# Performance work log

Hardware: AMD Instinct MI355X
Metric: run time of the kernel (lower is better)

The kernel has to match this reference:

```python
import jax, jax.numpy as jnp
import numpy as np

N, F_IN, F_OUT = 8192, 512, 256

def setup_inputs() -> dict:
    key = jax.random.key(0)
    kx, kW, ka = jax.random.split(key, 3)
    x = jax.random.normal(kx, (N, F_IN), dtype=jnp.float32)
    adj = jnp.ones((N, N), dtype=jnp.float32)  # accepted but unused by the original forward
    # nn.Linear(in, out, bias=False) stores weight as [out, in]
    W = jax.random.normal(kW, (F_OUT, F_IN), dtype=jnp.float32) * 0.02
    # nn.Linear(2*out, 1, bias=False) -> attention vector of length 2*F_OUT
    a = jax.random.normal(ka, (2 * F_OUT,), dtype=jnp.float32) * 0.02
    return {"x": x, "adj": adj, "W": W, "a": a}

def reference(x, adj, W, a):
    # h = W(x): [N, F_OUT]
    h = x @ W.T
    # Original concatenates [h_i, h_j] for all pairs (O(N^2 * 2F) memory) and
    # applies linear a. Since a is linear, e_ij = a1.h_i + a2.h_j -> broadcast add.
    a_src, a_dst = a[:F_OUT], a[F_OUT:]
    e = (h @ a_src)[:, None] + (h @ a_dst)[None, :]  # [N, N]
    attention = jax.nn.softmax(e, axis=1)             # row-wise over neighbors j
    h_prime = attention @ h                           # [N, F_OUT]
    return h_prime
```

## Files before the change

### kernel.cpp

```cpp
#include <hip/hip_runtime.h>
#include <math.h>

#define NN 8192
#define FIN 512
#define FOUT 256

__global__ __launch_bounds__(256) void gemm_xwT(const float* __restrict__ A,
                                                const float* __restrict__ B,
                                                float* __restrict__ C) {
    const int K = FIN;
    __shared__ float As[32][68];
    __shared__ float Bs[32][68];

    const int bx = blockIdx.x;
    const int by = blockIdx.y;
    const int tid = threadIdx.x;
    const int tx = tid & 15;
    const int ty = tid >> 4;

    const int lr = tid >> 3;
    const int lk = (tid & 7) << 2;

    const float* Ab = A + (size_t)(by * 64) * K;
    const float* Bb = B + (size_t)(bx * 64) * K;

    float acc[4][4] = {};

    for (int k0 = 0; k0 < K; k0 += 32) {
        float4 a0 = *(const float4*)(Ab + (size_t)lr * K + k0 + lk);
        float4 a1 = *(const float4*)(Ab + (size_t)(lr + 32) * K + k0 + lk);
        float4 b0 = *(const float4*)(Bb + (size_t)lr * K + k0 + lk);
        float4 b1 = *(const float4*)(Bb + (size_t)(lr + 32) * K + k0 + lk);
        __syncthreads();
        As[lk + 0][lr] = a0.x; As[lk + 1][lr] = a0.y;
        As[lk + 2][lr] = a0.z; As[lk + 3][lr] = a0.w;
        As[lk + 0][lr + 32] = a1.x; As[lk + 1][lr + 32] = a1.y;
        As[lk + 2][lr + 32] = a1.z; As[lk + 3][lr + 32] = a1.w;
        Bs[lk + 0][lr] = b0.x; Bs[lk + 1][lr] = b0.y;
        Bs[lk + 2][lr] = b0.z; Bs[lk + 3][lr] = b0.w;
        Bs[lk + 0][lr + 32] = b1.x; Bs[lk + 1][lr + 32] = b1.y;
        Bs[lk + 2][lr + 32] = b1.z; Bs[lk + 3][lr + 32] = b1.w;
        __syncthreads();
        #pragma unroll
        for (int kk = 0; kk < 32; ++kk) {
            float4 av = *(const float4*)&As[kk][ty << 2];
            float4 bv = *(const float4*)&Bs[kk][tx << 2];
            float am[4] = {av.x, av.y, av.z, av.w};
            float bn[4] = {bv.x, bv.y, bv.z, bv.w};
            #pragma unroll
            for (int i = 0; i < 4; ++i)
                #pragma unroll
                for (int j = 0; j < 4; ++j)
                    acc[i][j] = fmaf(am[i], bn[j], acc[i][j]);
        }
    }

    const int m0 = by * 64 + (ty << 2);
    const int n0 = bx * 64 + (tx << 2);
    #pragma unroll
    for (int i = 0; i < 4; ++i) {
        float4 o = make_float4(acc[i][0], acc[i][1], acc[i][2], acc[i][3]);
        *(float4*)(C + (size_t)(m0 + i) * FOUT + n0) = o;
    }
}

__global__ __launch_bounds__(256) void row_dot(const float* __restrict__ h,
                                               const float* __restrict__ a_dst,
                                               float* __restrict__ d) {
    const int lane = threadIdx.x & 63;
    const int wave = threadIdx.x >> 6;
    const int row = blockIdx.x * 4 + wave;
    float4 hv = *(const float4*)(h + (size_t)row * FOUT + (lane << 2));
    float4 av = *(const float4*)(a_dst + (lane << 2));
    float s = hv.x * av.x + hv.y * av.y + hv.z * av.z + hv.w * av.w;
    #pragma unroll
    for (int off = 32; off; off >>= 1) s += __shfl_down(s, off);
    if (lane == 0) d[row] = s;
}

__global__ __launch_bounds__(1024) void softmax_stats(const float* __restrict__ d,
                                                      float* __restrict__ stats) {
    __shared__ float red[16];
    const int tid = threadIdx.x;
    const int lane = tid & 63;
    const int wid = tid >> 6;

    const float4* dp = (const float4*)d + (size_t)tid * 2;
    float4 v0 = dp[0], v1 = dp[1];

    float m = fmaxf(fmaxf(fmaxf(v0.x, v0.y), fmaxf(v0.z, v0.w)),
                    fmaxf(fmaxf(v1.x, v1.y), fmaxf(v1.z, v1.w)));
    #pragma unroll
    for (int off = 32; off; off >>= 1) m = fmaxf(m, __shfl_xor(m, off));
    if (lane == 0) red[wid] = m;
    __syncthreads();
    if (tid == 0) {
        float mm = red[0];
        #pragma unroll
        for (int i = 1; i < 16; ++i) mm = fmaxf(mm, red[i]);
        red[0] = mm;
    }
    __syncthreads();
    const float M = red[0];
    __syncthreads();

    float s = expf(v0.x - M) + expf(v0.y - M) + expf(v0.z - M) + expf(v0.w - M)
            + expf(v1.x - M) + expf(v1.y - M) + expf(v1.z - M) + expf(v1.w - M);
    #pragma unroll
    for (int off = 32; off; off >>= 1) s += __shfl_xor(s, off);
    if (lane == 0) red[wid] = s;
    __syncthreads();
    if (tid == 0) {
        float ss = 0.f;
        #pragma unroll
        for (int i = 0; i < 16; ++i) ss += red[i];
        stats[0] = M;
        stats[1] = ss;
    }
}

__global__ __launch_bounds__(256) void weighted_sum(const float* __restrict__ h,
                                                    const float* __restrict__ d,
                                                    const float* __restrict__ stats,
                                                    float* __restrict__ v) {
    __shared__ float w[128];
    const int tid = threadIdx.x;
    const int r0 = blockIdx.x * 128;
    const float M = stats[0];
    if (tid < 128) w[tid] = expf(d[r0 + tid] - M);
    __syncthreads();
    float acc = 0.f;
    #pragma unroll 8
    for (int j = 0; j < 128; ++j)
        acc = fmaf(w[j], h[(size_t)(r0 + j) * FOUT + tid], acc);
    atomicAdd(&v[tid], acc);
}

__global__ __launch_bounds__(256) void broadcast_out(const float* __restrict__ v,
                                                     const float* __restrict__ stats,
                                                     float* __restrict__ out) {
    const int idx = blockIdx.x * 256 + threadIdx.x;
    const float inv = 1.0f / stats[1];
    float4 vv = ((const float4*)v)[idx & 63];
    vv.x *= inv; vv.y *= inv; vv.z *= inv; vv.w *= inv;
    ((float4*)out)[idx] = vv;
}

extern "C" void kernel_launch(void* const* d_in, const int* in_sizes, int n_in,
                              void* d_out, int out_size, void* d_ws, size_t ws_size,
                              hipStream_t stream) {
    const float* x = (const float*)d_in[0];
    const float* W = (const float*)d_in[2];
    const float* a = (const float*)d_in[3];
    float* out = (float*)d_out;

    float* ws    = (float*)d_ws;
    float* dvec  = ws;
    float* stats = ws + NN;
    float* v     = ws + NN + 16;

    hipMemsetAsync(v, 0, FOUT * sizeof(float), stream);

    gemm_xwT<<<dim3(FOUT / 64, NN / 64), 256, 0, stream>>>(x, W, out);
    row_dot<<<NN / 4, 256, 0, stream>>>(out, a + FOUT, dvec);
    softmax_stats<<<1, 1024, 0, stream>>>(dvec, stats);
    weighted_sum<<<NN / 128, 256, 0, stream>>>(out, dvec, stats, v);
    broadcast_out<<<(NN * FOUT / 4) / 256, 256, 0, stream>>>(v, stats, out);
}
```

Before: 358.6 us.

## Reassociate matmuls to avoid materializing h = xW^T

The N×F_OUT GEMM is replaced by algebraic reassociation. The per-row scores are computed as x·(W^T a_dst) via a small g-vector kernel and a row dot over x. The weighted sum is taken over x columns and then projected through W, and the zeroing of u is folded into the stats kernel, removing the memset. This drops the large GEMM and the write and re-read of h, but changes floating-point summation order.

```diff
diff --git a/kernel.cpp b/kernel.cpp
--- a/kernel.cpp
+++ b/kernel.cpp
@@ -5,85 +5,53 @@
 #define FIN 512
 #define FOUT 256
 
-__global__ __launch_bounds__(256) void gemm_xwT(const float* __restrict__ A,
-                                                const float* __restrict__ B,
-                                                float* __restrict__ C) {
-    const int K = FIN;
-    __shared__ float As[32][68];
-    __shared__ float Bs[32][68];
 
-    const int bx = blockIdx.x;
-    const int by = blockIdx.y;
+__global__ __launch_bounds__(256) void compute_g(const float* __restrict__ W,
+                                                 const float* __restrict__ a_dst,
+                                                 float* __restrict__ g) {
+    __shared__ float red[4][64];
     const int tid = threadIdx.x;
-    const int tx = tid & 15;
-    const int ty = tid >> 4;
-
-    const int lr = tid >> 3;
-    const int lk = (tid & 7) << 2;
-
-    const float* Ab = A + (size_t)(by * 64) * K;
-    const float* Bb = B + (size_t)(bx * 64) * K;
-
-    float acc[4][4] = {};
-
-    for (int k0 = 0; k0 < K; k0 += 32) {
-        float4 a0 = *(const float4*)(Ab + (size_t)lr * K + k0 + lk);
-        float4 a1 = *(const float4*)(Ab + (size_t)(lr + 32) * K + k0 + lk);
-        float4 b0 = *(const float4*)(Bb + (size_t)lr * K + k0 + lk);
-        float4 b1 = *(const float4*)(Bb + (size_t)(lr + 32) * K + k0 + lk);
-        __syncthreads();
-        As[lk + 0][lr] = a0.x; As[lk + 1][lr] = a0.y;
-        As[lk + 2][lr] = a0.z; As[lk + 3][lr] = a0.w;
-        As[lk + 0][lr + 32] = a1.x; As[lk + 1][lr + 32] = a1.y;
-        As[lk + 2][lr + 32] = a1.z; As[lk + 3][lr + 32] = a1.w;
-        Bs[lk + 0][lr] = b0.x; Bs[lk + 1][lr] = b0.y;
-        Bs[lk + 2][lr] = b0.z; Bs[lk + 3][lr] = b0.w;
-        Bs[lk + 0][lr + 32] = b1.x; Bs[lk + 1][lr + 32] = b1.y;
-        Bs[lk + 2][lr + 32] = b1.z; Bs[lk + 3][lr + 32] = b1.w;
-        __syncthreads();
-        #pragma unroll
-        for (int kk = 0; kk < 32; ++kk) {
-            float4 av = *(const float4*)&As[kk][ty << 2];
-            float4 bv = *(const float4*)&Bs[kk][tx << 2];
-            float am[4] = {av.x, av.y, av.z, av.w};
-            float bn[4] = {bv.x, bv.y, bv.z, bv.w};
-            #pragma unroll
-            for (int i = 0; i < 4; ++i)
-                #pragma unroll
-                for (int j = 0; j < 4; ++j)
-                    acc[i][j] = fmaf(am[i], bn[j], acc[i][j]);
-        }
-    }
-
-    const int m0 = by * 64 + (ty << 2);
-    const int n0 = bx * 64 + (tx << 2);
-    #pragma unroll
-    for (int i = 0; i < 4; ++i) {
-        float4 o = make_float4(acc[i][0], acc[i][1], acc[i][2], acc[i][3]);
-        *(float4*)(C + (size_t)(m0 + i) * FOUT + n0) = o;
-    }
+    const int kl = tid & 63;
+    const int cp = tid >> 6;
+    const int k = blockIdx.x * 64 + kl;
+    float s = 0.f;
+    #pragma unroll 8
+    for (int c = cp * 64; c < cp * 64 + 64; ++c)
+        s = fmaf(W[(size_t)c * FIN + k], a_dst[c], s);
+    red[cp][kl] = s;
+    __syncthreads();
+    if (cp == 0) g[k] = red[0][kl] + red[1][kl] + red[2][kl] + red[3][kl];
 }
 
-__global__ __launch_bounds__(256) void row_dot(const float* __restrict__ h,
-                                               const float* __restrict__ a_dst,
-                                               float* __restrict__ d) {
-    const int lane = threadIdx.x & 63;
-    const int wave = threadIdx.x >> 6;
+__global__ __launch_bounds__(256) void rowdot_xg(const float* __restrict__ x,
+                                                 const float* __restrict__ g,
+                                                 float* __restrict__ d) {
+    __shared__ float gs[FIN];
+    const int tid = threadIdx.x;
+    if (tid < 128) ((float4*)gs)[tid] = ((const float4*)g)[tid];
+    __syncthreads();
+    const int lane = tid & 63;
+    const int wave = tid >> 6;
     const int row = blockIdx.x * 4 + wave;
-    float4 hv = *(const float4*)(h + (size_t)row * FOUT + (lane << 2));
-    float4 av = *(const float4*)(a_dst + (lane << 2));
-    float s = hv.x * av.x + hv.y * av.y + hv.z * av.z + hv.w * av.w;
+    const float4* xr = (const float4*)(x + (size_t)row * FIN);
+    float4 x0 = xr[lane * 2], x1 = xr[lane * 2 + 1];
+    float4 g0 = ((const float4*)gs)[lane * 2], g1 = ((const float4*)gs)[lane * 2 + 1];
+    float s = x0.x * g0.x + x0.y * g0.y + x0.z * g0.z + x0.w * g0.w
+            + x1.x * g1.x + x1.y * g1.y + x1.z * g1.z + x1.w * g1.w;
     #pragma unroll
     for (int off = 32; off; off >>= 1) s += __shfl_down(s, off);
     if (lane == 0) d[row] = s;
 }
 
 __global__ __launch_bounds__(1024) void softmax_stats(const float* __restrict__ d,
-                                                      float* __restrict__ stats) {
+                                                      float* __restrict__ stats,
+                                                      float* __restrict__ u) {
     __shared__ float red[16];
     const int tid = threadIdx.x;
     const int lane = tid & 63;
     const int wid = tid >> 6;
+
+    if (tid < FIN) u[tid] = 0.f;
 
     const float4* dp = (const float4*)d + (size_t)tid * 2;
     float4 v0 = dp[0], v1 = dp[1];
@@ -119,10 +87,10 @@
     }
 }
 
-__global__ __launch_bounds__(256) void weighted_sum(const float* __restrict__ h,
-                                                    const float* __restrict__ d,
-                                                    const float* __restrict__ stats,
-                                                    float* __restrict__ v) {
+__global__ __launch_bounds__(512) void weighted_colsum(const float* __restrict__ x,
+                                                       const float* __restrict__ d,
+                                                       const float* __restrict__ stats,
+                                                       float* __restrict__ u) {
     __shared__ float w[128];
     const int tid = threadIdx.x;
     const int r0 = blockIdx.x * 128;
@@ -132,17 +100,35 @@
     float acc = 0.f;
     #pragma unroll 8
     for (int j = 0; j < 128; ++j)
-        acc = fmaf(w[j], h[(size_t)(r0 + j) * FOUT + tid], acc);
-    atomicAdd(&v[tid], acc);
+        acc = fmaf(w[j], x[(size_t)(r0 + j) * FIN + tid], acc);
+    atomicAdd(&u[tid], acc);
 }
 
-__global__ __launch_bounds__(256) void broadcast_out(const float* __restrict__ v,
-                                                     const float* __restrict__ stats,
+__global__ __launch_bounds__(256) void compute_v(const float* __restrict__ W,
+                                                 const float* __restrict__ u,
+                                                 const float* __restrict__ stats,
+                                                 float* __restrict__ vs) {
+    __shared__ float us[FIN];
+    const int tid = threadIdx.x;
+    if (tid < 128) ((float4*)us)[tid] = ((const float4*)u)[tid];
+    __syncthreads();
+    const int lane = tid & 63;
+    const int wave = tid >> 6;
+    const int c = blockIdx.x * 4 + wave;
+    const float4* wr = (const float4*)(W + (size_t)c * FIN);
+    float4 w0 = wr[lane * 2], w1 = wr[lane * 2 + 1];
+    float4 u0 = ((const float4*)us)[lane * 2], u1 = ((const float4*)us)[lane * 2 + 1];
+    float s = w0.x * u0.x + w0.y * u0.y + w0.z * u0.z + w0.w * u0.w
+            + w1.x * u1.x + w1.y * u1.y + w1.z * u1.z + w1.w * u1.w;
+    #pragma unroll
+    for (int off = 32; off; off >>= 1) s += __shfl_down(s, off);
+    if (lane == 0) vs[c] = s / stats[1];
+}
+
+__global__ __launch_bounds__(256) void broadcast_out(const float* __restrict__ vs,
                                                      float* __restrict__ out) {
     const int idx = blockIdx.x * 256 + threadIdx.x;
-    const float inv = 1.0f / stats[1];
-    float4 vv = ((const float4*)v)[idx & 63];
-    vv.x *= inv; vv.y *= inv; vv.z *= inv; vv.w *= inv;
+    float4 vv = ((const float4*)vs)[idx & 63];
     ((float4*)out)[idx] = vv;
 }
 
@@ -157,13 +143,14 @@
     float* ws    = (float*)d_ws;
     float* dvec  = ws;
     float* stats = ws + NN;
-    float* v     = ws + NN + 16;
+    float* g     = ws + NN + 16;
+    float* u     = ws + NN + 16 + 512;
+    float* vs    = ws + NN + 16 + 1024;
 
-    hipMemsetAsync(v, 0, FOUT * sizeof(float), stream);
-
-    gemm_xwT<<<dim3(FOUT / 64, NN / 64), 256, 0, stream>>>(x, W, out);
-    row_dot<<<NN / 4, 256, 0, stream>>>(out, a + FOUT, dvec);
-    softmax_stats<<<1, 1024, 0, stream>>>(dvec, stats);
-    weighted_sum<<<NN / 128, 256, 0, stream>>>(out, dvec, stats, v);
-    broadcast_out<<<(NN * FOUT / 4) / 256, 256, 0, stream>>>(v, stats, out);
+    compute_g<<<8, 256, 0, stream>>>(W, a + FOUT, g);
+    rowdot_xg<<<NN / 4, 256, 0, stream>>>(x, g, dvec);
+    softmax_stats<<<1, 1024, 0, stream>>>(dvec, stats, u);
+    weighted_colsum<<<NN / 128, 512, 0, stream>>>(x, dvec, stats, u);
+    compute_v<<<FOUT / 4, 256, 0, stream>>>(W, u, stats, vs);
+    broadcast_out<<<(NN * FOUT / 4) / 256, 256, 0, stream>>>(vs, out);
 }
```

Result: faster. 330.2 us (-7.9%).
